# Performance work log

Hardware: AMD Instinct MI355X
Metric: run time of the kernel (lower is better)

Reference implementation:

```python
import jax, jax.numpy as jnp
import numpy as np

NH, NKV, HD = 32, 8, 128      # query heads, kv heads, head dim
B, S, H = 4, 1024, 4096       # batch, per-seq tokens (prefill, no history), hidden
BLOCK = 64                    # paged KV-cache block size
BPS = S // BLOCK              # blocks per sequence


def rotate_half(x):
    x1, x2 = jnp.split(x, 2, axis=-1)
    return jnp.concatenate([-x2, x1], axis=-1)


def setup_inputs() -> dict:
    key = jax.random.key(0)
    ks = jax.random.split(key, 5)
    hidden_states = jax.random.normal(ks[0], (B * S, H), jnp.float32)
    Wq = jax.random.normal(ks[1], (H, NH * HD), jnp.float32) * 0.02
    Wk = jax.random.normal(ks[2], (H, NKV * HD), jnp.float32) * 0.02
    Wv = jax.random.normal(ks[3], (H, NKV * HD), jnp.float32) * 0.02
    Wo = jax.random.normal(ks[4], (NH * HD, H), jnp.float32) * 0.02
    # standard llama rope inverse frequencies
    inv_freq = 1.0 / (10000.0 ** (jnp.arange(0, HD, 2, dtype=jnp.float32) / HD))
    # empty paged KV cache: [num_blocks, block, n_kv_heads, head_dim]
    k_cache = jnp.zeros((B * BPS, BLOCK, NKV, HD), jnp.float32)
    v_cache = jnp.zeros((B * BPS, BLOCK, NKV, HD), jnp.float32)
    # per-token positions (prefill, history=0): 0..S-1 for each sequence
    position_ids_1d = jnp.tile(jnp.arange(S, dtype=jnp.int32), B)
    # block table: which cache block holds each logical block of each sequence
    block_offsets = jnp.arange(B * BPS, dtype=jnp.int32).reshape(B, BPS)
    return dict(hidden_states=hidden_states, Wq=Wq, Wk=Wk, Wv=Wv, Wo=Wo,
                inv_freq=inv_freq, k_cache=k_cache, v_cache=v_cache,
                position_ids_1d=position_ids_1d, block_offsets=block_offsets)


def reference(hidden_states, Wq, Wk, Wv, Wo, inv_freq, k_cache, v_cache,
              position_ids_1d, block_offsets):
    # qkv projections (contiguous-batching: tokens flattened)
    q = (hidden_states @ Wq).reshape(-1, NH, HD)
    k = (hidden_states @ Wk).reshape(-1, NKV, HD)
    v = (hidden_states @ Wv).reshape(-1, NKV, HD)

    # fused rotary: cos/sin from inv_freq at per-token 1d positions
    freqs = position_ids_1d.astype(jnp.float32)[:, None] * inv_freq[None, :]  # [T, HD/2]
    emb = jnp.concatenate([freqs, freqs], axis=-1)                            # [T, HD]
    cos = jnp.cos(emb)[:, None, :]
    sin = jnp.sin(emb)[:, None, :]
    q = q * cos + rotate_half(q) * sin
    k = k * cos + rotate_half(k) * sin

    # fill_kv_cache: scatter rotated K / raw V into paged cache via block_offsets
    flat_offsets = block_offsets.reshape(-1)
    k_blk = k.reshape(B * BPS, BLOCK, NKV, HD)
    v_blk = v.reshape(B * BPS, BLOCK, NKV, HD)
    k_cache = k_cache.at[flat_offsets].set(k_blk)
    v_cache = v_cache.at[flat_offsets].set(v_blk)

    # paged_attention_fwd: gather K/V blocks back via block table
    kk = k_cache[block_offsets].reshape(B, BPS * BLOCK, NKV, HD)  # [B, Skv, NKV, HD]
    vv = v_cache[block_offsets].reshape(B, BPS * BLOCK, NKV, HD)
    groups = NH // NKV
    kk = jnp.repeat(kk, groups, axis=2)  # repeat_kv -> [B, Skv, NH, HD]
    vv = jnp.repeat(vv, groups, axis=2)

    qb = q.reshape(B, S, NH, HD)
    scale = 1.0 / jnp.sqrt(jnp.float32(HD))
    scores = jnp.einsum('bqhd,bkhd->bhqk', qb, kk) * scale  # [B, NH, S, Skv]
    causal = jnp.arange(S)[:, None] >= jnp.arange(BPS * BLOCK)[None, :]
    scores = jnp.where(causal[None, None], scores, jnp.float32(-1e30))
    probs = jax.nn.softmax(scores, axis=-1)
    attn = jnp.einsum('bhqk,bkhd->bqhd', probs, vv).reshape(B * S, NH * HD)
    return attn @ Wo
```

## Files before the change

kernel.cpp:

```cpp
#include <hip/hip_runtime.h>
#include <cstdint>
#include <cstddef>


typedef unsigned short u16;
typedef __bf16 bf16x8 __attribute__((ext_vector_type(8)));
typedef float  f32x4  __attribute__((ext_vector_type(4)));

#define SEQ 1024
#define QKV_COLS 6144
#define NHEAD 32
#define NKVH 8
#define HDIM 128

__device__ __forceinline__ u16 f2bf(float f) {
  union { float f; uint32_t u; } v; v.f = f;
  return (u16)((v.u + 0x7fffu + ((v.u >> 16) & 1u)) >> 16);
}
__device__ __forceinline__ float bf2f(u16 x) {
  union { uint32_t u; float f; } v; v.u = ((uint32_t)x) << 16;
  return v.f;
}

typedef __attribute__((address_space(1))) const uint32_t g_u32;
typedef __attribute__((address_space(3))) uint32_t l_u32;
__device__ __forceinline__ void async_copy16(const u16* g, u16* lds_base) {
  __builtin_amdgcn_global_load_lds((g_u32*)g, (l_u32*)lds_base, 16, 0, 0);
}

__global__ void cast_f32_bf16(const float* __restrict__ in, u16* __restrict__ out, int n) {
  int i = (blockIdx.x * 256 + threadIdx.x) * 4;
  if (i >= n) return;
  float4 v = *(const float4*)&in[i];
  uint2 pk;
  pk.x = (uint32_t)f2bf(v.x) | ((uint32_t)f2bf(v.y) << 16);
  pk.y = (uint32_t)f2bf(v.z) | ((uint32_t)f2bf(v.w) << 16);
  *(uint2*)&out[i] = pk;
}

__global__ void transpose_f32_bf16(const float* __restrict__ in, u16* __restrict__ out,
                                   int R, int C) {
  __shared__ float tile[32][33];
  int c0 = blockIdx.x * 32, r0 = blockIdx.y * 32;
  int tx = threadIdx.x, ty = threadIdx.y;
  tile[ty][tx] = in[(size_t)(r0 + ty) * C + c0 + tx];
  __syncthreads();
  out[(size_t)(c0 + ty) * R + r0 + tx] = f2bf(tile[tx][ty]);
}

template <int MODE>
__global__ __launch_bounds__(512, 2) void gemm_bt(const u16* __restrict__ A,
                                                  const u16* __restrict__ Bt,
                                                  void* __restrict__ Cv,
                                                  u16* __restrict__ Vt,
                                                  const float* __restrict__ invf,
                                                  const int* __restrict__ pos,
                                                  int M, int N, int K, int ldc,
                                                  int nbx) {
  __shared__ __align__(16) u16 smem[4][2][256 * 32];

  const int tid = threadIdx.x;
  const int lane = tid & 63, wave = tid >> 6;
  const int l15 = lane & 15, qd = lane >> 4;
  const int wm = wave & 3, wn = wave >> 2;

  const int nwg = gridDim.x;
  const int bid = (int)blockIdx.x;
  const int swz = (bid & 7) * (nwg >> 3) + (bid >> 3);
  const int bx = swz % nbx, by = swz / nbx;
  const int row0 = by * 256, col0 = bx * 256;

  const int sl = (qd ^ (l15 & 3) ^ (l15 >> 2)) * 8;

  int soff[2], cb[2];
#pragma unroll
  for (int call = 0; call < 2; ++call) {
    const int c = call * 512 + tid;
    const int r = c >> 2, j = c & 3;
    const int src = j ^ (r & 3) ^ ((r >> 2) & 3);
    soff[call] = r * K + src * 8;
    cb[call] = (call * 512 + wave * 64) * 8;
  }

  const u16* Ab = A + (size_t)row0 * K;
  const u16* Bb = Bt + (size_t)col0 * K;
  const int NT = K >> 5;

  f32x4 acc[4][8] = {};

#pragma unroll
  for (int tt = 0; tt < 3; ++tt) {
#pragma unroll
    for (int call = 0; call < 2; ++call)
      async_copy16(&Ab[tt * 32 + soff[call]], &smem[tt][0][cb[call]]);
#pragma unroll
    for (int call = 0; call < 2; ++call)
      async_copy16(&Bb[tt * 32 + soff[call]], &smem[tt][1][cb[call]]);
  }
  asm volatile("s_waitcnt vmcnt(4)" ::: "memory");
  __builtin_amdgcn_s_barrier();
  asm volatile("" ::: "memory");

  bf16x8 a[4], b[4];
#pragma unroll
  for (int i = 0; i < 4; ++i) {
    a[i] = *(const bf16x8*)&smem[0][0][(wm * 64 + i * 16 + l15) * 32 + sl];
    b[i] = *(const bf16x8*)&smem[0][1][(wn * 128 + i * 16 + l15) * 32 + sl];
  }

#pragma unroll 2
  for (int t = 0; t < NT; ++t) {
    const int bsel = t & 3, nsel = (t + 1) & 3, ssel = (t + 3) & 3;
    const bool do_stage = (t + 3) < NT;
    const bool have_next = (t + 1) < NT;
    const int knext = (t + 3) * 32;
    const u16* Bsc = &smem[bsel][1][0];
    const u16* Asn = &smem[nsel][0][0];
    const u16* Bsn = &smem[nsel][1][0];

    bf16x8 bh[4];
#pragma unroll
    for (int i = 0; i < 4; ++i)
      bh[i] = *(const bf16x8*)&Bsc[(wn * 128 + (4 + i) * 16 + l15) * 32 + sl];
    if (do_stage) {
#pragma unroll
      for (int call = 0; call < 2; ++call)
        async_copy16(&Ab[knext + soff[call]], &smem[ssel][0][cb[call]]);
    }
    __builtin_amdgcn_sched_barrier(0);
    __builtin_amdgcn_s_setprio(1);
#pragma unroll
    for (int mi = 0; mi < 4; ++mi)
#pragma unroll
      for (int ni = 0; ni < 4; ++ni)
        acc[mi][ni] = __builtin_amdgcn_mfma_f32_16x16x32_bf16(a[mi], b[ni], acc[mi][ni], 0, 0, 0);
    __builtin_amdgcn_s_setprio(0);

    bf16x8 a2[4], b2[4];
    if (have_next) {
#pragma unroll
      for (int i = 0; i < 4; ++i) {
        a2[i] = *(const bf16x8*)&Asn[(wm * 64 + i * 16 + l15) * 32 + sl];
        b2[i] = *(const bf16x8*)&Bsn[(wn * 128 + i * 16 + l15) * 32 + sl];
      }
    }
    if (do_stage) {
#pragma unroll
      for (int call = 0; call < 2; ++call)
        async_copy16(&Bb[knext + soff[call]], &smem[ssel][1][cb[call]]);
    }
    __builtin_amdgcn_sched_barrier(0);
    __builtin_amdgcn_s_setprio(1);
#pragma unroll
    for (int mi = 0; mi < 4; ++mi)
#pragma unroll
      for (int ni = 0; ni < 4; ++ni)
        acc[mi][4 + ni] = __builtin_amdgcn_mfma_f32_16x16x32_bf16(a[mi], bh[ni], acc[mi][4 + ni], 0, 0, 0);
    __builtin_amdgcn_s_setprio(0);

    if (t < NT - 2) {
      if (t < NT - 3) asm volatile("s_waitcnt vmcnt(4)" ::: "memory");
      else            asm volatile("s_waitcnt vmcnt(0)" ::: "memory");
      __builtin_amdgcn_s_barrier();
      asm volatile("" ::: "memory");
    }
    if (have_next) {
#pragma unroll
      for (int i = 0; i < 4; ++i) { a[i] = a2[i]; b[i] = b2[i]; }
    }
  }

  if (MODE == 0 && col0 >= 5120) {
#pragma unroll
    for (int mi = 0; mi < 4; ++mi)
#pragma unroll
      for (int ni = 0; ni < 8; ++ni) {
        const int col = col0 + wn * 128 + ni * 16 + l15;
        const int dcol = col - 5120, kvh = dcol >> 7, d = dcol & 127;
        const int row = row0 + wm * 64 + mi * 16 + qd * 4;
        const int bb = row >> 10, p = row & 1023;
        ushort4 pk;
        pk.x = f2bf(acc[mi][ni][0]); pk.y = f2bf(acc[mi][ni][1]);
        pk.z = f2bf(acc[mi][ni][2]); pk.w = f2bf(acc[mi][ni][3]);
        *(ushort4*)&Vt[(((size_t)(bb * 8 + kvh) * 128) + d) * 1024 + p] = pk;
      }
    return;
  }
  if (MODE == 0) {
    const int c0w = col0 + wn * 128;
    float fi[4];
#pragma unroll
    for (int ni = 0; ni < 4; ++ni) fi[ni] = invf[ni * 16 + l15];
    u16* C16 = (u16*)Cv;
#pragma unroll
    for (int mi = 0; mi < 4; ++mi) {
      const int rbase = row0 + wm * 64 + mi * 16 + qd * 4;
#pragma unroll
      for (int r = 0; r < 4; ++r) {
        const float pv = (float)pos[rbase + r];
        const size_t rowoff = (size_t)(rbase + r) * ldc + c0w;
#pragma unroll
        for (int ni = 0; ni < 4; ++ni) {
          const float x1 = acc[mi][ni][r], x2 = acc[mi][ni + 4][r];
          float s, c;
          __sincosf(pv * fi[ni], &s, &c);
          C16[rowoff + ni * 16 + l15]      = f2bf(x1 * c - x2 * s);
          C16[rowoff + 64 + ni * 16 + l15] = f2bf(x2 * c + x1 * s);
        }
      }
    }
    return;
  }
#pragma unroll
  for (int mi = 0; mi < 4; ++mi)
#pragma unroll
    for (int ni = 0; ni < 8; ++ni)
#pragma unroll
      for (int r = 0; r < 4; ++r) {
        int row = row0 + wm * 64 + mi * 16 + qd * 4 + r;
        int col = col0 + wn * 128 + ni * 16 + l15;
        ((float*)Cv)[(size_t)row * ldc + col] = acc[mi][ni][r];
      }
}

__global__ __launch_bounds__(512, 4) void attn_kernel(const u16* __restrict__ qkv,
                                                      const u16* __restrict__ vt,
                                                      u16* __restrict__ ao) {
  __shared__ __align__(16) u16 Ks[64 * 136];
  __shared__ __align__(16) u16 Vts[128 * 68];
  __shared__ __align__(16) u16 Ps[8][16 * 68];

  const int tid = threadIdx.x;
  const int lane = tid & 63, wave = tid >> 6;
  const int l15 = lane & 15, qd = lane >> 4;
  const int qt = blockIdx.x, h = blockIdx.y, b = blockIdx.z;
  const int q0 = qt * 128;
  const int kvh = h >> 2;
  const float scale = 0.08838834764831845f;

  bf16x8 qf[4];
  {
    const size_t qrow = (size_t)(b * SEQ + q0 + wave * 16 + l15) * QKV_COLS + h * HDIM;
#pragma unroll
    for (int s = 0; s < 4; ++s) qf[s] = *(const bf16x8*)&qkv[qrow + s * 32 + qd * 8];
  }

  f32x4 o[8] = {};
  float mrow[4] = {-__builtin_inff(), -__builtin_inff(), -__builtin_inff(), -__builtin_inff()};
  float lrow[4] = {0.f, 0.f, 0.f, 0.f};

  const int nkt = qt * 2 + 2;
  const size_t vbase0 = ((size_t)(b * NKVH + kvh) * HDIM) * SEQ;
  for (int kt = 0; kt < nkt; ++kt) {
    const int kv0 = kt * 64;
#pragma unroll
    for (int rnd = 0; rnd < 2; ++rnd) {
      int c = tid + rnd * 512;
      int kv = c >> 4, dc = (c & 15) * 8;
      *(uint4*)&Ks[kv * 136 + dc] =
          *(const uint4*)&qkv[(size_t)(b * SEQ + kv0 + kv) * QKV_COLS + 4096 + kvh * HDIM + dc];
    }
#pragma unroll
    for (int rnd = 0; rnd < 2; ++rnd) {
      int c = tid + rnd * 512;
      int d = c >> 3, kc = (c & 7) * 8;
      *(uint4*)&Vts[d * 68 + kc] = *(const uint4*)&vt[vbase0 + (size_t)d * SEQ + kv0 + kc];
    }
    __syncthreads();

    f32x4 st[4] = {};
#pragma unroll
    for (int t = 0; t < 4; ++t)
#pragma unroll
      for (int s = 0; s < 4; ++s) {
        bf16x8 kf = *(const bf16x8*)&Ks[(t * 16 + l15) * 136 + s * 32 + qd * 8];
        st[t] = __builtin_amdgcn_mfma_f32_16x16x32_bf16(qf[s], kf, st[t], 0, 0, 0);
      }

    float al[4];
#pragma unroll
    for (int r = 0; r < 4; ++r) {
      const int qpos = q0 + wave * 16 + qd * 4 + r;
      float sc[4];
#pragma unroll
      for (int t = 0; t < 4; ++t) {
        sc[t] = st[t][r] * scale;
        if (kv0 + t * 16 + l15 > qpos) sc[t] = -1e30f;
      }
      float mt = fmaxf(fmaxf(sc[0], sc[1]), fmaxf(sc[2], sc[3]));
      mt = fmaxf(mt, __shfl_xor(mt, 8));
      mt = fmaxf(mt, __shfl_xor(mt, 4));
      mt = fmaxf(mt, __shfl_xor(mt, 2));
      mt = fmaxf(mt, __shfl_xor(mt, 1));
      const float mn = fmaxf(mrow[r], mt);
      al[r] = __expf(mrow[r] - mn);
      float p[4], rs = 0.f;
#pragma unroll
      for (int t = 0; t < 4; ++t) { p[t] = __expf(sc[t] - mn); rs += p[t]; }
      rs += __shfl_xor(rs, 8);
      rs += __shfl_xor(rs, 4);
      rs += __shfl_xor(rs, 2);
      rs += __shfl_xor(rs, 1);
      lrow[r] = lrow[r] * al[r] + rs;
      mrow[r] = mn;
#pragma unroll
      for (int t = 0; t < 4; ++t)
        Ps[wave][(qd * 4 + r) * 68 + t * 16 + l15] = f2bf(p[t]);
    }
    asm volatile("s_waitcnt lgkmcnt(0)" ::: "memory");

    {
      const int srcl = (l15 >> 2) * 16;
      float a0 = __shfl(al[0], srcl), a1 = __shfl(al[1], srcl);
      float a2 = __shfl(al[2], srcl), a3 = __shfl(al[3], srcl);
      const int rr = l15 & 3;
      float aq = (rr & 2) ? ((rr & 1) ? a3 : a2) : ((rr & 1) ? a1 : a0);
#pragma unroll
      for (int dt = 0; dt < 8; ++dt) o[dt] *= aq;
    }
    {
      const bf16x8 pf0 = *(const bf16x8*)&Ps[wave][l15 * 68 + qd * 8];
      const bf16x8 pf1 = *(const bf16x8*)&Ps[wave][l15 * 68 + 32 + qd * 8];
#pragma unroll
      for (int dt = 0; dt < 8; ++dt) {
        const bf16x8 vf0 = *(const bf16x8*)&Vts[(dt * 16 + l15) * 68 + qd * 8];
        const bf16x8 vf1 = *(const bf16x8*)&Vts[(dt * 16 + l15) * 68 + 32 + qd * 8];
        o[dt] = __builtin_amdgcn_mfma_f32_16x16x32_bf16(vf0, pf0, o[dt], 0, 0, 0);
        o[dt] = __builtin_amdgcn_mfma_f32_16x16x32_bf16(vf1, pf1, o[dt], 0, 0, 0);
      }
    }
    __syncthreads();
  }

  {
    const int srcl = (l15 >> 2) * 16;
    float l0 = __shfl(lrow[0], srcl), l1 = __shfl(lrow[1], srcl);
    float l2 = __shfl(lrow[2], srcl), l3 = __shfl(lrow[3], srcl);
    const int rr = l15 & 3;
    float lq = (rr & 2) ? ((rr & 1) ? l3 : l2) : ((rr & 1) ? l1 : l0);
    const float inv = 1.0f / lq;
    const size_t obase = (size_t)(b * SEQ + q0 + wave * 16 + l15) * (NHEAD * HDIM) + h * HDIM;
#pragma unroll
    for (int dt = 0; dt < 8; ++dt) {
      ushort4 pk;
      pk.x = f2bf(o[dt][0] * inv); pk.y = f2bf(o[dt][1] * inv);
      pk.z = f2bf(o[dt][2] * inv); pk.w = f2bf(o[dt][3] * inv);
      *(ushort4*)&ao[obase + dt * 16 + qd * 4] = pk;
    }
  }
}

extern "C" void kernel_launch(void* const* d_in, const int* in_sizes, int n_in,
                              void* d_out, int out_size, void* d_ws, size_t ws_size,
                              hipStream_t stream) {
  const float* X    = (const float*)d_in[0];
  const float* Wq   = (const float*)d_in[1];
  const float* Wk   = (const float*)d_in[2];
  const float* Wv   = (const float*)d_in[3];
  const float* Wo   = (const float*)d_in[4];
  const float* invf = (const float*)d_in[5];
  const int*   pos  = (const int*)d_in[8];
  float* out = (float*)d_out;

  char* ws = (char*)d_ws;
  u16* Xbf   = (u16*)(ws + 0);
  u16* Wqkvt = (u16*)(ws + 33554432);
  u16* Wot   = (u16*)(ws + 83886080);
  u16* QKV   = (u16*)(ws + 117440512);
  u16* Vt    = (u16*)(ws + 167772160);
  u16* AO    = Xbf;

  dim3 tb32(32, 32);
  cast_f32_bf16<<<16384, 256, 0, stream>>>(X, Xbf, 16777216);
  transpose_f32_bf16<<<dim3(128, 128), tb32, 0, stream>>>(Wq, Wqkvt, 4096, 4096);
  transpose_f32_bf16<<<dim3(32, 128),  tb32, 0, stream>>>(Wk, Wqkvt + (size_t)4096 * 4096, 4096, 1024);
  transpose_f32_bf16<<<dim3(32, 128),  tb32, 0, stream>>>(Wv, Wqkvt + (size_t)5120 * 4096, 4096, 1024);
  transpose_f32_bf16<<<dim3(128, 128), tb32, 0, stream>>>(Wo, Wot, 4096, 4096);

  gemm_bt<0><<<dim3(24 * 16), 512, 0, stream>>>(Xbf, Wqkvt, QKV, Vt, invf, pos,
                                                4096, 6144, 4096, 6144, 24);
  attn_kernel<<<dim3(8, 32, 4), 512, 0, stream>>>(QKV, Vt, AO);
  gemm_bt<1><<<dim3(16 * 16), 512, 0, stream>>>(AO, Wot, out, Vt, nullptr, nullptr,
                                                4096, 4096, 4096, 4096, 16);
}
```

Before: 805.8 us.

## Switch GEMM inner loop from 16x16x32 to 32x32x16 bf16 MFMA tiles

Rewrites the GEMM microkernel to use 32x32x16 bf16 MFMA instructions with 16-wide accumulators instead of 16x16x32 ones. The shared-memory fragment loads, swizzle offsets and all epilogues (RoPE, V transpose, fp32 output) are remapped to the 32x32 output layout. The larger MFMA shape is meant to cut LDS fragment reads and instruction count per flop. It changes the register layout and the store patterns, which risks less coalesced epilogue writes and different register pressure.

```diff
diff --git a/kernel.cpp b/kernel.cpp
--- a/kernel.cpp
+++ b/kernel.cpp
@@ -6,6 +6,7 @@
 typedef unsigned short u16;
 typedef __bf16 bf16x8 __attribute__((ext_vector_type(8)));
 typedef float  f32x4  __attribute__((ext_vector_type(4)));
+typedef float  f32x16 __attribute__((ext_vector_type(16)));
 
 #define SEQ 1024
 #define QKV_COLS 6144
@@ -61,7 +62,7 @@
 
   const int tid = threadIdx.x;
   const int lane = tid & 63, wave = tid >> 6;
-  const int l15 = lane & 15, qd = lane >> 4;
+  const int l31 = lane & 31, hi = lane >> 5;
   const int wm = wave & 3, wn = wave >> 2;
 
   const int nwg = gridDim.x;
@@ -70,32 +71,34 @@
   const int bx = swz % nbx, by = swz / nbx;
   const int row0 = by * 256, col0 = bx * 256;
 
-  const int sl = (qd ^ (l15 & 3) ^ (l15 >> 2)) * 8;
-
-  int soff[2], cb[2];
+  const int s_l = (lane & 3) ^ ((l31 >> 2) & 3);
+  const int off0 = ((0 * 2 + hi) ^ s_l) * 8;
+  const int off1 = ((1 * 2 + hi) ^ s_l) * 8;
+
+  int soff[2], cb2[2];
 #pragma unroll
   for (int call = 0; call < 2; ++call) {
     const int c = call * 512 + tid;
     const int r = c >> 2, j = c & 3;
     const int src = j ^ (r & 3) ^ ((r >> 2) & 3);
     soff[call] = r * K + src * 8;
-    cb[call] = (call * 512 + wave * 64) * 8;
+    cb2[call] = (call * 512 + wave * 64) * 8;
   }
 
   const u16* Ab = A + (size_t)row0 * K;
   const u16* Bb = Bt + (size_t)col0 * K;
   const int NT = K >> 5;
 
-  f32x4 acc[4][8] = {};
+  f32x16 acc[2][4] = {};
 
 #pragma unroll
   for (int tt = 0; tt < 3; ++tt) {
 #pragma unroll
     for (int call = 0; call < 2; ++call)
-      async_copy16(&Ab[tt * 32 + soff[call]], &smem[tt][0][cb[call]]);
+      async_copy16(&Ab[tt * 32 + soff[call]], &smem[tt][0][cb2[call]]);
 #pragma unroll
     for (int call = 0; call < 2; ++call)
-      async_copy16(&Bb[tt * 32 + soff[call]], &smem[tt][1][cb[call]]);
+      async_copy16(&Bb[tt * 32 + soff[call]], &smem[tt][1][cb2[call]]);
   }
   asm volatile("s_waitcnt vmcnt(4)" ::: "memory");
   __builtin_amdgcn_s_barrier();
@@ -103,9 +106,14 @@
 
   bf16x8 a[4], b[4];
 #pragma unroll
-  for (int i = 0; i < 4; ++i) {
-    a[i] = *(const bf16x8*)&smem[0][0][(wm * 64 + i * 16 + l15) * 32 + sl];
-    b[i] = *(const bf16x8*)&smem[0][1][(wn * 128 + i * 16 + l15) * 32 + sl];
+  for (int rb = 0; rb < 2; ++rb) {
+    a[rb * 2 + 0] = *(const bf16x8*)&smem[0][0][(wm * 64 + rb * 32 + l31) * 32 + off0];
+    a[rb * 2 + 1] = *(const bf16x8*)&smem[0][0][(wm * 64 + rb * 32 + l31) * 32 + off1];
+  }
+#pragma unroll
+  for (int cb = 0; cb < 2; ++cb) {
+    b[cb * 2 + 0] = *(const bf16x8*)&smem[0][1][(wn * 128 + cb * 32 + l31) * 32 + off0];
+    b[cb * 2 + 1] = *(const bf16x8*)&smem[0][1][(wn * 128 + cb * 32 + l31) * 32 + off1];
   }
 
 #pragma unroll 2
@@ -120,42 +128,55 @@
 
     bf16x8 bh[4];
 #pragma unroll
-    for (int i = 0; i < 4; ++i)
-      bh[i] = *(const bf16x8*)&Bsc[(wn * 128 + (4 + i) * 16 + l15) * 32 + sl];
+    for (int cb = 0; cb < 2; ++cb) {
+      bh[cb * 2 + 0] = *(const bf16x8*)&Bsc[(wn * 128 + (2 + cb) * 32 + l31) * 32 + off0];
+      bh[cb * 2 + 1] = *(const bf16x8*)&Bsc[(wn * 128 + (2 + cb) * 32 + l31) * 32 + off1];
+    }
     if (do_stage) {
 #pragma unroll
       for (int call = 0; call < 2; ++call)
-        async_copy16(&Ab[knext + soff[call]], &smem[ssel][0][cb[call]]);
+        async_copy16(&Ab[knext + soff[call]], &smem[ssel][0][cb2[call]]);
     }
     __builtin_amdgcn_sched_barrier(0);
     __builtin_amdgcn_s_setprio(1);
 #pragma unroll
-    for (int mi = 0; mi < 4; ++mi)
-#pragma unroll
-      for (int ni = 0; ni < 4; ++ni)
-        acc[mi][ni] = __builtin_amdgcn_mfma_f32_16x16x32_bf16(a[mi], b[ni], acc[mi][ni], 0, 0, 0);
+    for (int rb = 0; rb < 2; ++rb)
+#pragma unroll
+      for (int cb = 0; cb < 2; ++cb)
+#pragma unroll
+        for (int ks = 0; ks < 2; ++ks)
+          acc[rb][cb] = __builtin_amdgcn_mfma_f32_32x32x16_bf16(
+              a[rb * 2 + ks], b[cb * 2 + ks], acc[rb][cb], 0, 0, 0);
     __builtin_amdgcn_s_setprio(0);
 
     bf16x8 a2[4], b2[4];
     if (have_next) {
 #pragma unroll
-      for (int i = 0; i < 4; ++i) {
-        a2[i] = *(const bf16x8*)&Asn[(wm * 64 + i * 16 + l15) * 32 + sl];
-        b2[i] = *(const bf16x8*)&Bsn[(wn * 128 + i * 16 + l15) * 32 + sl];
+      for (int rb = 0; rb < 2; ++rb) {
+        a2[rb * 2 + 0] = *(const bf16x8*)&Asn[(wm * 64 + rb * 32 + l31) * 32 + off0];
+        a2[rb * 2 + 1] = *(const bf16x8*)&Asn[(wm * 64 + rb * 32 + l31) * 32 + off1];
+      }
+#pragma unroll
+      for (int cb = 0; cb < 2; ++cb) {
+        b2[cb * 2 + 0] = *(const bf16x8*)&Bsn[(wn * 128 + cb * 32 + l31) * 32 + off0];
+        b2[cb * 2 + 1] = *(const bf16x8*)&Bsn[(wn * 128 + cb * 32 + l31) * 32 + off1];
       }
     }
     if (do_stage) {
 #pragma unroll
       for (int call = 0; call < 2; ++call)
-        async_copy16(&Bb[knext + soff[call]], &smem[ssel][1][cb[call]]);
+        async_copy16(&Bb[knext + soff[call]], &smem[ssel][1][cb2[call]]);
     }
     __builtin_amdgcn_sched_barrier(0);
     __builtin_amdgcn_s_setprio(1);
 #pragma unroll
-    for (int mi = 0; mi < 4; ++mi)
-#pragma unroll
-      for (int ni = 0; ni < 4; ++ni)
-        acc[mi][4 + ni] = __builtin_amdgcn_mfma_f32_16x16x32_bf16(a[mi], bh[ni], acc[mi][4 + ni], 0, 0, 0);
+    for (int rb = 0; rb < 2; ++rb)
+#pragma unroll
+      for (int cb = 0; cb < 2; ++cb)
+#pragma unroll
+        for (int ks = 0; ks < 2; ++ks)
+          acc[rb][2 + cb] = __builtin_amdgcn_mfma_f32_32x32x16_bf16(
+              a[rb * 2 + ks], bh[cb * 2 + ks], acc[rb][2 + cb], 0, 0, 0);
     __builtin_amdgcn_s_setprio(0);
 
     if (t < NT - 2) {
@@ -172,55 +193,63 @@
 
   if (MODE == 0 && col0 >= 5120) {
 #pragma unroll
-    for (int mi = 0; mi < 4; ++mi)
-#pragma unroll
-      for (int ni = 0; ni < 8; ++ni) {
-        const int col = col0 + wn * 128 + ni * 16 + l15;
+    for (int rb = 0; rb < 2; ++rb)
+#pragma unroll
+      for (int cb = 0; cb < 4; ++cb) {
+        const int col = col0 + wn * 128 + cb * 32 + l31;
         const int dcol = col - 5120, kvh = dcol >> 7, d = dcol & 127;
-        const int row = row0 + wm * 64 + mi * 16 + qd * 4;
-        const int bb = row >> 10, p = row & 1023;
-        ushort4 pk;
-        pk.x = f2bf(acc[mi][ni][0]); pk.y = f2bf(acc[mi][ni][1]);
-        pk.z = f2bf(acc[mi][ni][2]); pk.w = f2bf(acc[mi][ni][3]);
-        *(ushort4*)&Vt[(((size_t)(bb * 8 + kvh) * 128) + d) * 1024 + p] = pk;
+        const int rbase = row0 + wm * 64 + rb * 32 + hi * 4;
+        u16* vdst = &Vt[(((size_t)((rbase >> 10) * 8 + kvh) * 128) + d) * 1024];
+#pragma unroll
+        for (int q = 0; q < 4; ++q) {
+          const int p = (rbase + q * 8) & 1023;
+          ushort4 pk;
+          pk.x = f2bf(acc[rb][cb][q * 4 + 0]); pk.y = f2bf(acc[rb][cb][q * 4 + 1]);
+          pk.z = f2bf(acc[rb][cb][q * 4 + 2]); pk.w = f2bf(acc[rb][cb][q * 4 + 3]);
+          *(ushort4*)&vdst[p] = pk;
+        }
       }
     return;
   }
   if (MODE == 0) {
     const int c0w = col0 + wn * 128;
-    float fi[4];
-#pragma unroll
-    for (int ni = 0; ni < 4; ++ni) fi[ni] = invf[ni * 16 + l15];
+    const float f0 = invf[l31], f1 = invf[32 + l31];
     u16* C16 = (u16*)Cv;
 #pragma unroll
-    for (int mi = 0; mi < 4; ++mi) {
-      const int rbase = row0 + wm * 64 + mi * 16 + qd * 4;
-#pragma unroll
-      for (int r = 0; r < 4; ++r) {
-        const float pv = (float)pos[rbase + r];
-        const size_t rowoff = (size_t)(rbase + r) * ldc + c0w;
-#pragma unroll
-        for (int ni = 0; ni < 4; ++ni) {
-          const float x1 = acc[mi][ni][r], x2 = acc[mi][ni + 4][r];
-          float s, c;
-          __sincosf(pv * fi[ni], &s, &c);
-          C16[rowoff + ni * 16 + l15]      = f2bf(x1 * c - x2 * s);
-          C16[rowoff + 64 + ni * 16 + l15] = f2bf(x2 * c + x1 * s);
+    for (int rb = 0; rb < 2; ++rb) {
+      const int rbase = row0 + wm * 64 + rb * 32 + hi * 4;
+#pragma unroll
+      for (int q = 0; q < 4; ++q)
+#pragma unroll
+        for (int rr = 0; rr < 4; ++rr) {
+          const int reg = q * 4 + rr;
+          const int row = rbase + q * 8 + rr;
+          const float pv = (float)pos[row];
+          const size_t rowoff = (size_t)row * ldc + c0w;
+#pragma unroll
+          for (int cb = 0; cb < 2; ++cb) {
+            const float x1 = acc[rb][cb][reg], x2 = acc[rb][cb + 2][reg];
+            float s, c;
+            __sincosf(pv * (cb ? f1 : f0), &s, &c);
+            C16[rowoff + cb * 32 + l31]      = f2bf(x1 * c - x2 * s);
+            C16[rowoff + 64 + cb * 32 + l31] = f2bf(x2 * c + x1 * s);
+          }
         }
-      }
     }
     return;
   }
 #pragma unroll
-  for (int mi = 0; mi < 4; ++mi)
-#pragma unroll
-    for (int ni = 0; ni < 8; ++ni)
-#pragma unroll
-      for (int r = 0; r < 4; ++r) {
-        int row = row0 + wm * 64 + mi * 16 + qd * 4 + r;
-        int col = col0 + wn * 128 + ni * 16 + l15;
-        ((float*)Cv)[(size_t)row * ldc + col] = acc[mi][ni][r];
-      }
+  for (int rb = 0; rb < 2; ++rb)
+#pragma unroll
+    for (int cb = 0; cb < 4; ++cb) {
+      const int col = col0 + wn * 128 + cb * 32 + l31;
+      const int rbase = row0 + wm * 64 + rb * 32 + hi * 4;
+#pragma unroll
+      for (int q = 0; q < 4; ++q)
+#pragma unroll
+        for (int rr = 0; rr < 4; ++rr)
+          ((float*)Cv)[(size_t)(rbase + q * 8 + rr) * ldc + col] = acc[rb][cb][q * 4 + rr];
+    }
 }
 
 __global__ __launch_bounds__(512, 4) void attn_kernel(const u16* __restrict__ qkv,
```

Result: slower. 844.2 us (+4.8%).
